# Performance work log

Measured on AMD Instinct MI355X. Metric: run time of the kernel, lower is better.

Reference implementation:

```python
import jax, jax.numpy as jnp
import numpy as np

EPS = 1e-8

def rms_norm(x, scale):
    # full RMSNorm over last dim (p < 0 branch): norm/sqrt(d)
    d = x.shape[-1]
    norm = jnp.linalg.norm(x, ord=2, axis=-1, keepdims=True)
    rms = norm * (d ** -0.5)
    return scale * (x / (rms + EPS))

def setup_inputs() -> dict:
    key = jax.random.key(0)
    ks = jax.random.split(key, 4)
    B, N, C, H = 2, 2048, 1024, 16
    hd = C // H
    x = jax.random.normal(ks[0], (B, N, C), dtype=jnp.float32)
    Wqkv = jax.random.normal(ks[1], (C, 3 * C), dtype=jnp.float32) * (C ** -0.5)
    Wproj = jax.random.normal(ks[2], (C, C), dtype=jnp.float32) * (C ** -0.5)
    bproj = jnp.zeros((C,), dtype=jnp.float32)
    q_scale = jnp.ones((hd,), dtype=jnp.float32)
    k_scale = jnp.ones((hd,), dtype=jnp.float32)
    return {"x": x, "Wqkv": Wqkv, "Wproj": Wproj, "bproj": bproj,
            "q_scale": q_scale, "k_scale": k_scale}

def reference(x, Wqkv, Wproj, bproj, q_scale, k_scale):
    B, N, C = x.shape
    H = 16
    hd = C // H
    scale = hd ** -0.5
    qkv = (x @ Wqkv).reshape(B, N, 3, H, hd)
    qkv = jnp.transpose(qkv, (2, 0, 3, 1, 4))  # t b h n c
    q, k, v = qkv[0], qkv[1], qkv[2]
    q = rms_norm(q, q_scale)
    k = rms_norm(k, k_scale)
    attn = jnp.einsum('bhnc,bhmc->bhnm', q, k) * scale
    attn = jax.nn.softmax(attn, axis=-1)
    out = jnp.einsum('bhnm,bhmc->bhnc', attn, v)
    out = jnp.transpose(out, (0, 2, 1, 3)).reshape(B, N, C)
    return out @ Wproj + bproj
```

## Files before the change

kernel.cpp:

```cpp
#include <hip/hip_runtime.h>


typedef _Float16 half_t;
typedef __attribute__((ext_vector_type(2))) __fp16 fp16x2;
typedef __attribute__((ext_vector_type(4))) _Float16 half4v;
typedef __attribute__((ext_vector_type(8))) _Float16 half8;
typedef __attribute__((ext_vector_type(4))) float f32x4;

#define DI __device__ __forceinline__

DI void gl_lds16(const void* g, void* l) {
    __builtin_amdgcn_global_load_lds((const __attribute__((address_space(1))) void*)g,
                                     (__attribute__((address_space(3))) void*)l, 16, 0, 0);
}

DI float exp2_fast(float x) {
    float r;
    asm("v_exp_f32 %0, %1" : "=v"(r) : "v"(x));
    return r;
}


__global__ void prep_x(const float* __restrict__ x, half_t* __restrict__ xh, int n) {
    int i = (blockIdx.x * 256 + threadIdx.x) * 4;
    if (i >= n) return;
    float4 v = *(const float4*)(x + i);
    half4v o;
    o[0] = (half_t)v.x; o[1] = (half_t)v.y; o[2] = (half_t)v.z; o[3] = (half_t)v.w;
    *(half4v*)(xh + i) = o;
}

__global__ void prep_wqkv(const float* __restrict__ w, half_t* __restrict__ wt) {
    __shared__ float t[32][33];
    int c0 = blockIdx.x * 32, r0 = blockIdx.y * 32;
    int tx = threadIdx.x, ty = threadIdx.y;
#pragma unroll
    for (int i = 0; i < 4; i++)
        t[ty + 8 * i][tx] = w[(size_t)(r0 + ty + 8 * i) * 3072 + c0 + tx];
    __syncthreads();
#pragma unroll
    for (int i = 0; i < 4; i++)
        wt[(size_t)(c0 + ty + 8 * i) * 1024 + r0 + tx] = (half_t)t[tx][ty + 8 * i];
}

__global__ void prep_wproj(const float* __restrict__ w, half_t* __restrict__ wt) {
    __shared__ float t[32][33];
    int c0 = blockIdx.x * 32, r0 = blockIdx.y * 32;
    int tx = threadIdx.x, ty = threadIdx.y;
#pragma unroll
    for (int i = 0; i < 4; i++)
        t[ty + 8 * i][tx] = w[(size_t)(r0 + ty + 8 * i) * 1024 + c0 + tx];
    __syncthreads();
#pragma unroll
    for (int i = 0; i < 4; i++)
        wt[(size_t)(c0 + ty + 8 * i) * 1024 + r0 + tx] = (half_t)t[tx][ty + 8 * i];
}

__global__ __launch_bounds__(256) void gemm_qkv(
    const half_t* __restrict__ A, const half_t* __restrict__ Bt,
    half_t* __restrict__ qh, half_t* __restrict__ kh, half_t* __restrict__ vth) {
    const int K = 1024;
    __shared__ __align__(16) half_t Al[2][128 * 64];
    __shared__ __align__(16) half_t Bl[2][128 * 64];
    int tid = threadIdx.x;
    int w = tid >> 6, l = tid & 63;
    int wr = w >> 1, wc = w & 1;
    int g = l >> 4, r = l & 15;
    int m0 = blockIdx.x * 128, n0 = blockIdx.y * 128;
    f32x4 acc[4][4] = {};

#define STAGE_QKV(kt, buf)                                                        \
    {                                                                             \
        _Pragma("unroll")                                                         \
        for (int p = 0; p < 4; p++) {                                             \
            int ci = p * 256 + tid;                                               \
            int row = ci >> 3, c = ci & 7, lc = c ^ (row & 7);                    \
            gl_lds16(A + (size_t)(m0 + row) * K + (kt) * 64 + lc * 8,             \
                     &Al[buf][0] + ci * 8);                                       \
            gl_lds16(Bt + (size_t)(n0 + row) * K + (kt) * 64 + lc * 8,            \
                     &Bl[buf][0] + ci * 8);                                       \
        }                                                                         \
    }

    STAGE_QKV(0, 0);
    __syncthreads();
    int cur = 0;
    for (int kt = 0; kt < 16; kt++) {
        if (kt < 15) STAGE_QKV(kt + 1, cur ^ 1);
#pragma unroll
        for (int ks = 0; ks < 2; ks++) {
            half8 af[4], bf[4];
#pragma unroll
            for (int i = 0; i < 4; i++) {
                int row = wr * 64 + i * 16 + r;
                af[i] = *(const half8*)(&Al[cur][0] + row * 64 + (((4 * ks + g) ^ (row & 7)) << 3));
                int rowb = wc * 64 + i * 16 + r;
                bf[i] = *(const half8*)(&Bl[cur][0] + rowb * 64 + (((4 * ks + g) ^ (rowb & 7)) << 3));
            }
#pragma unroll
            for (int i = 0; i < 4; i++)
#pragma unroll
                for (int j = 0; j < 4; j++)
                    acc[i][j] = __builtin_amdgcn_mfma_f32_16x16x32_f16(af[i], bf[j], acc[i][j], 0, 0, 0);
        }
        __syncthreads();
        cur ^= 1;
    }

#pragma unroll
    for (int i = 0; i < 4; i++)
#pragma unroll
        for (int j = 0; j < 4; j++) {
            int gcol = n0 + wc * 64 + j * 16 + r;
            int t = gcol >> 10;
            int h = (gcol >> 6) & 15;
            int f = gcol & 63;
            int growb = m0 + wr * 64 + i * 16 + g * 4;
            int b = growb >> 11;
            int n = growb & 2047;
            int bh = b * 16 + h;
            if (t == 2) {
                half4v pv;
#pragma unroll
                for (int rr = 0; rr < 4; rr++) pv[rr] = (half_t)acc[i][j][rr];
                *(half4v*)(vth + ((size_t)bh * 64 + f) * 2048 + n) = pv;
            } else {
                half_t* dst = (t == 0 ? qh : kh);
#pragma unroll
                for (int rr = 0; rr < 4; rr++)
                    dst[((size_t)bh * 2048 + n + rr) * 64 + f] = (half_t)acc[i][j][rr];
            }
        }
}

__global__ void rmsnorm_qk(half_t* __restrict__ qh, half_t* __restrict__ kh,
                           const float* __restrict__ qs, const float* __restrict__ ks2) {
    int tid = blockIdx.x * 256 + threadIdx.x;
    int row = tid >> 4;
    int lq = tid & 15;
    bool isq = row < 65536;
    half_t* base = isq ? (qh + (size_t)row * 64) : (kh + (size_t)(row - 65536) * 64);
    const float* sc = isq ? qs : ks2;
    float extra = isq ? (0.125f * 1.44269504f) : 1.0f;
    half4v v = *(half4v*)(base + lq * 4);
    float f0 = (float)v[0], f1 = (float)v[1], f2 = (float)v[2], f3 = (float)v[3];
    float ss = f0 * f0 + f1 * f1 + f2 * f2 + f3 * f3;
#pragma unroll
    for (int d = 1; d < 16; d <<= 1) ss += __shfl_xor(ss, d, 64);
    float rms = sqrtf(ss) * 0.125f;
    float inv = extra / (rms + 1e-8f);
    half4v o;
    o[0] = (half_t)(f0 * sc[lq * 4 + 0] * inv);
    o[1] = (half_t)(f1 * sc[lq * 4 + 1] * inv);
    o[2] = (half_t)(f2 * sc[lq * 4 + 2] * inv);
    o[3] = (half_t)(f3 * sc[lq * 4 + 3] * inv);
    *(half4v*)(base + lq * 4) = o;
}

__global__ __launch_bounds__(512) void attn(
    const half_t* __restrict__ qh, const half_t* __restrict__ kh,
    const half_t* __restrict__ vth, half_t* __restrict__ aoh) {
    int bh = blockIdx.y;
    int q0 = blockIdx.x * 128;
    const half_t* Qp = qh + (size_t)bh * 2048 * 64;
    const half_t* Kp = kh + (size_t)bh * 2048 * 64;
    const half_t* Vp = vth + (size_t)bh * 64 * 2048;
    __shared__ __align__(16) half_t Kl[2][64 * 64];
    __shared__ __align__(16) half_t Vl[2][64 * 64];
    __shared__ __align__(16) half_t Pl[8][16 * 64];
    int tid = threadIdx.x, w = tid >> 6, l = tid & 63, g = l >> 4, r = l & 15;

    int srow = tid >> 3, sc = tid & 7, slc = sc ^ (srow & 7);

    half8 qf[2];
#pragma unroll
    for (int ks = 0; ks < 2; ks++)
        qf[ks] = *(const half8*)(Qp + (size_t)(q0 + w * 16 + r) * 64 + ks * 32 + g * 8);

    f32x4 o[4] = {};
    float m = -1e30f, lsum = 0.f;

    gl_lds16(Kp + (size_t)srow * 64 + slc * 8, &Kl[0][0] + tid * 8);
    gl_lds16(Vp + (size_t)srow * 2048 + slc * 8, &Vl[0][0] + tid * 8);
    __syncthreads();

    int cur = 0;
    for (int t = 0; t < 32; t++) {
        if (t < 31) {
            int kv1 = (t + 1) * 64;
            gl_lds16(Kp + (size_t)(kv1 + srow) * 64 + slc * 8, &Kl[cur ^ 1][0] + tid * 8);
            gl_lds16(Vp + (size_t)srow * 2048 + kv1 + slc * 8, &Vl[cur ^ 1][0] + tid * 8);
        }
        const half_t* Kc = &Kl[cur][0];
        const half_t* Vc = &Vl[cur][0];

        f32x4 s[4] = {};
#pragma unroll
        for (int ks = 0; ks < 2; ks++)
#pragma unroll
            for (int tt = 0; tt < 4; tt++) {
                int row = tt * 16 + r;
                half8 kf = *(const half8*)(Kc + row * 64 + (((4 * ks + g) ^ (row & 7)) << 3));
                s[tt] = __builtin_amdgcn_mfma_f32_16x16x32_f16(kf, qf[ks], s[tt], 0, 0, 0);
            }

        float mx = -1e30f;
#pragma unroll
        for (int tt = 0; tt < 4; tt++)
            mx = fmaxf(mx, fmaxf(fmaxf(s[tt][0], s[tt][1]), fmaxf(s[tt][2], s[tt][3])));
        mx = fmaxf(mx, __shfl_xor(mx, 16, 64));
        mx = fmaxf(mx, __shfl_xor(mx, 32, 64));
        if (!__all(mx <= m + 11.0f)) {
            float mn = fmaxf(m, mx);
            float fac = exp2_fast(m - mn);
            lsum *= fac;
#pragma unroll
            for (int cf = 0; cf < 4; cf++) {
                o[cf][0] *= fac; o[cf][1] *= fac; o[cf][2] *= fac; o[cf][3] *= fac;
            }
            m = mn;
        }
        float rs = 0.f;
#pragma unroll
        for (int tt = 0; tt < 4; tt++)
#pragma unroll
            for (int e = 0; e < 4; e++) {
                float p = exp2_fast(s[tt][e] - m);
                s[tt][e] = p;
                rs += p;
            }
        rs += __shfl_xor(rs, 16, 64);
        rs += __shfl_xor(rs, 32, 64);
        lsum += rs;

        half_t* Pw = &Pl[w][0];
#pragma unroll
        for (int tt = 0; tt < 4; tt++) {
            fp16x2 a = __builtin_amdgcn_cvt_pkrtz(s[tt][0], s[tt][1]);
            fp16x2 b = __builtin_amdgcn_cvt_pkrtz(s[tt][2], s[tt][3]);
            half4v v4;
            v4[0] = (half_t)a[0]; v4[1] = (half_t)a[1];
            v4[2] = (half_t)b[0]; v4[3] = (half_t)b[1];
            *(half4v*)(Pw + r * 64 + (((2 * tt + (g >> 1)) ^ (r & 7)) << 3) + ((2 * g) & 3) * 2) = v4;
        }

#pragma unroll
        for (int ks2 = 0; ks2 < 2; ks2++) {
            half8 pf = *(const half8*)(Pw + r * 64 + (((4 * ks2 + g) ^ (r & 7)) << 3));
#pragma unroll
            for (int cf = 0; cf < 4; cf++) {
                int row = cf * 16 + r;
                half8 vf = *(const half8*)(Vc + row * 64 + (((4 * ks2 + g) ^ (row & 7)) << 3));
                o[cf] = __builtin_amdgcn_mfma_f32_16x16x32_f16(vf, pf, o[cf], 0, 0, 0);
            }
        }
        __syncthreads();
        cur ^= 1;
    }

    int b = bh >> 4, h = bh & 15;
    int n = q0 + w * 16 + r;
    float inv = 1.0f / lsum;
#pragma unroll
    for (int cf = 0; cf < 4; cf++) {
        half4v ov;
#pragma unroll
        for (int reg = 0; reg < 4; reg++) ov[reg] = (half_t)(o[cf][reg] * inv);
        *(half4v*)(aoh + ((size_t)b * 2048 + n) * 1024 + h * 64 + cf * 16 + g * 4) = ov;
    }
}

__global__ __launch_bounds__(256) void gemm_proj(
    const half_t* __restrict__ A, const half_t* __restrict__ Bt,
    const float* __restrict__ bias, float* __restrict__ out) {
    const int K = 1024;
    __shared__ __align__(16) half_t Al[128 * 64];
    __shared__ __align__(16) half_t Bl[128 * 64];
    int tid = threadIdx.x, w = tid >> 6, l = tid & 63;
    int wr = w >> 1, wc = w & 1, g = l >> 4, r = l & 15;
    int m0 = blockIdx.x * 128, n0 = blockIdx.y * 128;
    f32x4 acc[4][4] = {};

    for (int k0 = 0; k0 < K; k0 += 64) {
#pragma unroll
        for (int p = 0; p < 4; p++) {
            int ci = (p * 4 + w) * 64 + l;
            int row = ci >> 3, c = ci & 7;
            int lc = c ^ (row & 7);
            gl_lds16(A + (size_t)(m0 + row) * K + k0 + lc * 8, Al + (p * 4 + w) * 512);
            gl_lds16(Bt + (size_t)(n0 + row) * K + k0 + lc * 8, Bl + (p * 4 + w) * 512);
        }
        __syncthreads();
#pragma unroll
        for (int ks = 0; ks < 2; ks++) {
            half8 af[4], bf[4];
#pragma unroll
            for (int i = 0; i < 4; i++) {
                int row = wr * 64 + i * 16 + r;
                af[i] = *(const half8*)(Al + row * 64 + (((4 * ks + g) ^ (row & 7)) << 3));
                int rowb = wc * 64 + i * 16 + r;
                bf[i] = *(const half8*)(Bl + rowb * 64 + (((4 * ks + g) ^ (rowb & 7)) << 3));
            }
#pragma unroll
            for (int i = 0; i < 4; i++)
#pragma unroll
                for (int j = 0; j < 4; j++)
                    acc[i][j] = __builtin_amdgcn_mfma_f32_16x16x32_f16(af[i], bf[j], acc[i][j], 0, 0, 0);
        }
        __syncthreads();
    }

#pragma unroll
    for (int i = 0; i < 4; i++)
#pragma unroll
        for (int j = 0; j < 4; j++) {
            int gcol = n0 + wc * 64 + j * 16 + r;
            float bv = bias[gcol];
#pragma unroll
            for (int rr = 0; rr < 4; rr++) {
                int grow = m0 + wr * 64 + i * 16 + g * 4 + rr;
                out[(size_t)grow * 1024 + gcol] = acc[i][j][rr] + bv;
            }
        }
}

extern "C" void kernel_launch(void* const* d_in, const int* in_sizes, int n_in,
                              void* d_out, int out_size, void* d_ws, size_t ws_size,
                              hipStream_t stream) {
    const float* x = (const float*)d_in[0];
    const float* Wqkv = (const float*)d_in[1];
    const float* Wproj = (const float*)d_in[2];
    const float* bproj = (const float*)d_in[3];
    const float* qscale = (const float*)d_in[4];
    const float* kscale = (const float*)d_in[5];
    float* out = (float*)d_out;

    char* ws = (char*)d_ws;
    half_t* xh  = (half_t*)(ws + 0);
    half_t* wqt = (half_t*)(ws + 8388608);
    half_t* wpt = (half_t*)(ws + 14680064);
    half_t* qh  = (half_t*)(ws + 16777216);
    half_t* kh  = (half_t*)(ws + 25165824);
    half_t* vth = (half_t*)(ws + 33554432);
    half_t* aoh = (half_t*)(ws + 41943040);

    prep_x<<<4096, 256, 0, stream>>>(x, xh, 4194304);
    prep_wqkv<<<dim3(96, 32), dim3(32, 8), 0, stream>>>(Wqkv, wqt);
    prep_wproj<<<dim3(32, 32), dim3(32, 8), 0, stream>>>(Wproj, wpt);
    gemm_qkv<<<dim3(32, 24), 256, 0, stream>>>(xh, wqt, qh, kh, vth);
    rmsnorm_qk<<<8192, 256, 0, stream>>>(qh, kh, qscale, kscale);
    attn<<<dim3(16, 32), 512, 0, stream>>>(qh, kh, vth, aoh);
    gemm_proj<<<dim3(32, 8), 256, 0, stream>>>(aoh, wpt, bproj, out);
}
```

Measured before the change: 152.9 us.

## Fuse q/k RMSNorm into QKV GEMM epilogue and unroll attention loop

```diff
diff --git a/kernel.cpp b/kernel.cpp
--- a/kernel.cpp
+++ b/kernel.cpp
@@ -58,6 +58,7 @@
 
 __global__ __launch_bounds__(256) void gemm_qkv(
     const half_t* __restrict__ A, const half_t* __restrict__ Bt,
+    const float* __restrict__ qs, const float* __restrict__ ks,
     half_t* __restrict__ qh, half_t* __restrict__ kh, half_t* __restrict__ vth) {
     const int K = 1024;
     __shared__ __align__(16) half_t Al[2][128 * 64];
@@ -88,14 +89,14 @@
     for (int kt = 0; kt < 16; kt++) {
         if (kt < 15) STAGE_QKV(kt + 1, cur ^ 1);
 #pragma unroll
-        for (int ks = 0; ks < 2; ks++) {
+        for (int ks2 = 0; ks2 < 2; ks2++) {
             half8 af[4], bf[4];
 #pragma unroll
             for (int i = 0; i < 4; i++) {
                 int row = wr * 64 + i * 16 + r;
-                af[i] = *(const half8*)(&Al[cur][0] + row * 64 + (((4 * ks + g) ^ (row & 7)) << 3));
+                af[i] = *(const half8*)(&Al[cur][0] + row * 64 + (((4 * ks2 + g) ^ (row & 7)) << 3));
                 int rowb = wc * 64 + i * 16 + r;
-                bf[i] = *(const half8*)(&Bl[cur][0] + rowb * 64 + (((4 * ks + g) ^ (rowb & 7)) << 3));
+                bf[i] = *(const half8*)(&Bl[cur][0] + rowb * 64 + (((4 * ks2 + g) ^ (rowb & 7)) << 3));
             }
 #pragma unroll
             for (int i = 0; i < 4; i++)
@@ -107,57 +108,56 @@
         cur ^= 1;
     }
 
-#pragma unroll
-    for (int i = 0; i < 4; i++)
-#pragma unroll
-        for (int j = 0; j < 4; j++) {
-            int gcol = n0 + wc * 64 + j * 16 + r;
-            int t = gcol >> 10;
-            int h = (gcol >> 6) & 15;
-            int f = gcol & 63;
-            int growb = m0 + wr * 64 + i * 16 + g * 4;
-            int b = growb >> 11;
-            int n = growb & 2047;
-            int bh = b * 16 + h;
-            if (t == 2) {
+    int tsec = n0 >> 10;
+    if (tsec == 2) {
+#pragma unroll
+        for (int i = 0; i < 4; i++)
+#pragma unroll
+            for (int j = 0; j < 4; j++) {
+                int gcol = n0 + wc * 64 + j * 16 + r;
+                int h = (gcol >> 6) & 15;
+                int f = gcol & 63;
+                int growb = m0 + wr * 64 + i * 16 + g * 4;
+                int b = growb >> 11;
+                int n = growb & 2047;
                 half4v pv;
 #pragma unroll
                 for (int rr = 0; rr < 4; rr++) pv[rr] = (half_t)acc[i][j][rr];
-                *(half4v*)(vth + ((size_t)bh * 64 + f) * 2048 + n) = pv;
-            } else {
-                half_t* dst = (t == 0 ? qh : kh);
-#pragma unroll
-                for (int rr = 0; rr < 4; rr++)
-                    dst[((size_t)bh * 2048 + n + rr) * 64 + f] = (half_t)acc[i][j][rr];
-            }
-        }
-}
-
-__global__ void rmsnorm_qk(half_t* __restrict__ qh, half_t* __restrict__ kh,
-                           const float* __restrict__ qs, const float* __restrict__ ks2) {
-    int tid = blockIdx.x * 256 + threadIdx.x;
-    int row = tid >> 4;
-    int lq = tid & 15;
-    bool isq = row < 65536;
-    half_t* base = isq ? (qh + (size_t)row * 64) : (kh + (size_t)(row - 65536) * 64);
-    const float* sc = isq ? qs : ks2;
-    float extra = isq ? (0.125f * 1.44269504f) : 1.0f;
-    half4v v = *(half4v*)(base + lq * 4);
-    float f0 = (float)v[0], f1 = (float)v[1], f2 = (float)v[2], f3 = (float)v[3];
-    float ss = f0 * f0 + f1 * f1 + f2 * f2 + f3 * f3;
-#pragma unroll
-    for (int d = 1; d < 16; d <<= 1) ss += __shfl_xor(ss, d, 64);
-    float rms = sqrtf(ss) * 0.125f;
-    float inv = extra / (rms + 1e-8f);
-    half4v o;
-    o[0] = (half_t)(f0 * sc[lq * 4 + 0] * inv);
-    o[1] = (half_t)(f1 * sc[lq * 4 + 1] * inv);
-    o[2] = (half_t)(f2 * sc[lq * 4 + 2] * inv);
-    o[3] = (half_t)(f3 * sc[lq * 4 + 3] * inv);
-    *(half4v*)(base + lq * 4) = o;
-}
-
-__global__ __launch_bounds__(512) void attn(
+                *(half4v*)(vth + ((size_t)(b * 16 + h) * 64 + f) * 2048 + n) = pv;
+            }
+    } else {
+        const float* sc = (tsec == 0) ? qs : ks;
+        half_t* dst = (tsec == 0) ? qh : kh;
+        float extra = (tsec == 0) ? (0.125f * 1.44269504f) : 1.0f;
+        float scv[4];
+#pragma unroll
+        for (int j = 0; j < 4; j++) scv[j] = sc[j * 16 + r];
+#pragma unroll
+        for (int i = 0; i < 4; i++)
+#pragma unroll
+            for (int rr = 0; rr < 4; rr++) {
+                float ss = 0.f;
+#pragma unroll
+                for (int j = 0; j < 4; j++) ss += acc[i][j][rr] * acc[i][j][rr];
+#pragma unroll
+                for (int d = 1; d < 16; d <<= 1) ss += __shfl_xor(ss, d, 64);
+                float inv = extra / (sqrtf(ss) * 0.125f + 1e-8f);
+                int grow = m0 + wr * 64 + i * 16 + g * 4 + rr;
+                int b = grow >> 11;
+                int n = grow & 2047;
+#pragma unroll
+                for (int j = 0; j < 4; j++) {
+                    int gcol = n0 + wc * 64 + j * 16 + r;
+                    int h = (gcol >> 6) & 15;
+                    int f = gcol & 63;
+                    dst[((size_t)(b * 16 + h) * 2048 + n) * 64 + f] =
+                        (half_t)(acc[i][j][rr] * inv * scv[j]);
+                }
+            }
+    }
+}
+
+__global__ __launch_bounds__(512, 4) void attn(
     const half_t* __restrict__ qh, const half_t* __restrict__ kh,
     const half_t* __restrict__ vth, half_t* __restrict__ aoh) {
     int bh = blockIdx.y;
@@ -171,6 +171,31 @@
     int tid = threadIdx.x, w = tid >> 6, l = tid & 63, g = l >> 4, r = l & 15;
 
     int srow = tid >> 3, sc = tid & 7, slc = sc ^ (srow & 7);
+    const half_t* kst = Kp + (size_t)srow * 64 + slc * 8;
+    const half_t* vst = Vp + (size_t)srow * 2048 + slc * 8;
+
+    int koff[8], voff[8], poffw[4], poffr[2];
+#pragma unroll
+    for (int ks = 0; ks < 2; ks++)
+#pragma unroll
+        for (int tt = 0; tt < 4; tt++) {
+            int row = tt * 16 + r;
+            koff[ks * 4 + tt] = row * 64 + (((4 * ks + g) ^ (row & 7)) << 3);
+        }
+#pragma unroll
+    for (int ks2 = 0; ks2 < 2; ks2++)
+#pragma unroll
+        for (int cf = 0; cf < 4; cf++) {
+            int row = cf * 16 + r;
+            voff[ks2 * 4 + cf] = row * 64 + (((4 * ks2 + g) ^ (row & 7)) << 3);
+        }
+#pragma unroll
+    for (int tt = 0; tt < 4; tt++)
+        poffw[tt] = r * 64 + (((2 * tt + (g >> 1)) ^ (r & 7)) << 3) + (g & 1) * 4;
+#pragma unroll
+    for (int ks2 = 0; ks2 < 2; ks2++)
+        poffr[ks2] = r * 64 + (((4 * ks2 + g) ^ (r & 7)) << 3);
+    half_t* Pw = &Pl[w][0];
 
     half8 qf[2];
 #pragma unroll
@@ -180,82 +205,78 @@
     f32x4 o[4] = {};
     float m = -1e30f, lsum = 0.f;
 
-    gl_lds16(Kp + (size_t)srow * 64 + slc * 8, &Kl[0][0] + tid * 8);
-    gl_lds16(Vp + (size_t)srow * 2048 + slc * 8, &Vl[0][0] + tid * 8);
+    gl_lds16(kst, &Kl[0][0] + tid * 8);
+    gl_lds16(vst, &Vl[0][0] + tid * 8);
     __syncthreads();
 
-    int cur = 0;
-    for (int t = 0; t < 32; t++) {
-        if (t < 31) {
-            int kv1 = (t + 1) * 64;
-            gl_lds16(Kp + (size_t)(kv1 + srow) * 64 + slc * 8, &Kl[cur ^ 1][0] + tid * 8);
-            gl_lds16(Vp + (size_t)srow * 2048 + kv1 + slc * 8, &Vl[cur ^ 1][0] + tid * 8);
-        }
-        const half_t* Kc = &Kl[cur][0];
-        const half_t* Vc = &Vl[cur][0];
-
-        f32x4 s[4] = {};
-#pragma unroll
-        for (int ks = 0; ks < 2; ks++)
-#pragma unroll
-            for (int tt = 0; tt < 4; tt++) {
-                int row = tt * 16 + r;
-                half8 kf = *(const half8*)(Kc + row * 64 + (((4 * ks + g) ^ (row & 7)) << 3));
-                s[tt] = __builtin_amdgcn_mfma_f32_16x16x32_f16(kf, qf[ks], s[tt], 0, 0, 0);
-            }
-
-        float mx = -1e30f;
-#pragma unroll
-        for (int tt = 0; tt < 4; tt++)
-            mx = fmaxf(mx, fmaxf(fmaxf(s[tt][0], s[tt][1]), fmaxf(s[tt][2], s[tt][3])));
-        mx = fmaxf(mx, __shfl_xor(mx, 16, 64));
-        mx = fmaxf(mx, __shfl_xor(mx, 32, 64));
-        if (!__all(mx <= m + 11.0f)) {
-            float mn = fmaxf(m, mx);
-            float fac = exp2_fast(m - mn);
-            lsum *= fac;
-#pragma unroll
-            for (int cf = 0; cf < 4; cf++) {
-                o[cf][0] *= fac; o[cf][1] *= fac; o[cf][2] *= fac; o[cf][3] *= fac;
-            }
-            m = mn;
-        }
-        float rs = 0.f;
-#pragma unroll
-        for (int tt = 0; tt < 4; tt++)
-#pragma unroll
-            for (int e = 0; e < 4; e++) {
-                float p = exp2_fast(s[tt][e] - m);
-                s[tt][e] = p;
-                rs += p;
-            }
-        rs += __shfl_xor(rs, 16, 64);
-        rs += __shfl_xor(rs, 32, 64);
-        lsum += rs;
-
-        half_t* Pw = &Pl[w][0];
-#pragma unroll
-        for (int tt = 0; tt < 4; tt++) {
-            fp16x2 a = __builtin_amdgcn_cvt_pkrtz(s[tt][0], s[tt][1]);
-            fp16x2 b = __builtin_amdgcn_cvt_pkrtz(s[tt][2], s[tt][3]);
-            half4v v4;
-            v4[0] = (half_t)a[0]; v4[1] = (half_t)a[1];
-            v4[2] = (half_t)b[0]; v4[3] = (half_t)b[1];
-            *(half4v*)(Pw + r * 64 + (((2 * tt + (g >> 1)) ^ (r & 7)) << 3) + ((2 * g) & 3) * 2) = v4;
-        }
-
-#pragma unroll
-        for (int ks2 = 0; ks2 < 2; ks2++) {
-            half8 pf = *(const half8*)(Pw + r * 64 + (((4 * ks2 + g) ^ (r & 7)) << 3));
-#pragma unroll
-            for (int cf = 0; cf < 4; cf++) {
-                int row = cf * 16 + r;
-                half8 vf = *(const half8*)(Vc + row * 64 + (((4 * ks2 + g) ^ (row & 7)) << 3));
-                o[cf] = __builtin_amdgcn_mfma_f32_16x16x32_f16(vf, pf, o[cf], 0, 0, 0);
-            }
-        }
-        __syncthreads();
-        cur ^= 1;
+#define ATTN_TILE(BUF, T)                                                          \
+    {                                                                              \
+        if ((T) < 31) {                                                            \
+            gl_lds16(kst + ((T) + 1) * 4096, &Kl[(BUF) ^ 1][0] + tid * 8);         \
+            gl_lds16(vst + ((T) + 1) * 64, &Vl[(BUF) ^ 1][0] + tid * 8);           \
+        }                                                                          \
+        const half_t* Kc = &Kl[BUF][0];                                            \
+        const half_t* Vc = &Vl[BUF][0];                                            \
+        f32x4 s[4] = {};                                                           \
+        _Pragma("unroll")                                                          \
+        for (int ks = 0; ks < 2; ks++)                                             \
+            _Pragma("unroll")                                                      \
+            for (int tt = 0; tt < 4; tt++) {                                       \
+                half8 kf = *(const half8*)(Kc + koff[ks * 4 + tt]);                \
+                s[tt] = __builtin_amdgcn_mfma_f32_16x16x32_f16(kf, qf[ks], s[tt], 0, 0, 0); \
+            }                                                                      \
+        float mx = -1e30f;                                                         \
+        _Pragma("unroll")                                                          \
+        for (int tt = 0; tt < 4; tt++)                                             \
+            mx = fmaxf(mx, fmaxf(fmaxf(s[tt][0], s[tt][1]), fmaxf(s[tt][2], s[tt][3]))); \
+        mx = fmaxf(mx, __shfl_xor(mx, 16, 64));                                    \
+        mx = fmaxf(mx, __shfl_xor(mx, 32, 64));                                    \
+        if (!__all(mx <= m + 11.0f)) {                                             \
+            float mn = fmaxf(m, mx);                                               \
+            float fac = exp2_fast(m - mn);                                         \
+            lsum *= fac;                                                           \
+            _Pragma("unroll")                                                      \
+            for (int cf = 0; cf < 4; cf++) {                                       \
+                o[cf][0] *= fac; o[cf][1] *= fac; o[cf][2] *= fac; o[cf][3] *= fac; \
+            }                                                                      \
+            m = mn;                                                                \
+        }                                                                          \
+        float rs = 0.f;                                                            \
+        _Pragma("unroll")                                                          \
+        for (int tt = 0; tt < 4; tt++)                                             \
+            _Pragma("unroll")                                                      \
+            for (int e = 0; e < 4; e++) {                                          \
+                float p = exp2_fast(s[tt][e] - m);                                 \
+                s[tt][e] = p;                                                      \
+                rs += p;                                                           \
+            }                                                                      \
+        rs += __shfl_xor(rs, 16, 64);                                              \
+        rs += __shfl_xor(rs, 32, 64);                                              \
+        lsum += rs;                                                                \
+        _Pragma("unroll")                                                          \
+        for (int tt = 0; tt < 4; tt++) {                                           \
+            fp16x2 a = __builtin_amdgcn_cvt_pkrtz(s[tt][0], s[tt][1]);             \
+            fp16x2 b = __builtin_amdgcn_cvt_pkrtz(s[tt][2], s[tt][3]);             \
+            half4v v4;                                                             \
+            v4[0] = (half_t)a[0]; v4[1] = (half_t)a[1];                            \
+            v4[2] = (half_t)b[0]; v4[3] = (half_t)b[1];                            \
+            *(half4v*)(Pw + poffw[tt]) = v4;                                       \
+        }                                                                          \
+        _Pragma("unroll")                                                          \
+        for (int ks2 = 0; ks2 < 2; ks2++) {                                        \
+            half8 pf = *(const half8*)(Pw + poffr[ks2]);                           \
+            _Pragma("unroll")                                                      \
+            for (int cf = 0; cf < 4; cf++) {                                       \
+                half8 vf = *(const half8*)(Vc + voff[ks2 * 4 + cf]);               \
+                o[cf] = __builtin_amdgcn_mfma_f32_16x16x32_f16(vf, pf, o[cf], 0, 0, 0); \
+            }                                                                      \
+        }                                                                          \
+        __syncthreads();                                                           \
+    }
+
+    for (int t = 0; t < 32; t += 2) {
+        ATTN_TILE(0, t);
+        ATTN_TILE(1, t + 1);
     }
 
     int b = bh >> 4, h = bh & 15;
@@ -347,8 +368,7 @@
     prep_x<<<4096, 256, 0, stream>>>(x, xh, 4194304);
     prep_wqkv<<<dim3(96, 32), dim3(32, 8), 0, stream>>>(Wqkv, wqt);
     prep_wproj<<<dim3(32, 32), dim3(32, 8), 0, stream>>>(Wproj, wpt);
-    gemm_qkv<<<dim3(32, 24), 256, 0, stream>>>(xh, wqt, qh, kh, vth);
-    rmsnorm_qk<<<8192, 256, 0, stream>>>(qh, kh, qscale, kscale);
+    gemm_qkv<<<dim3(32, 24), 256, 0, stream>>>(xh, wqt, qscale, kscale, qh, kh, vth);
     attn<<<dim3(16, 32), 512, 0, stream>>>(qh, kh, vth, aoh);
     gemm_proj<<<dim3(32, 8), 256, 0, stream>>>(aoh, wpt, bproj, out);
 }
```

After: 138.4 us. 9.5% less time.
